# Kernel optimization log

Measured on AMD Instinct MI355X. Metric: run time of the kernel, lower is better.

## Reference

```python
import jax, jax.numpy as jnp
import numpy as np

N_ENT = 50000
N_USR = 10000
N_NODES = N_ENT + N_USR
D = 64            # entity_dim
AE_H = [128, 32]  # autoencoder hidden dims
CONV = [32, 16]   # graph conv output dims
R = 16            # n_relations
E = 1920000       # n_edges (avg degree 32)
B = 4096          # scoring batch


def setup_inputs() -> dict:
    key = jax.random.key(0)
    ks = jax.random.split(key, 24)
    s = 0.05
    rn = lambda k, shp: jax.random.normal(k, shp, jnp.float32) * s
    inp = {
        # int graph / batch inputs
        "users": jax.random.randint(ks[0], (B,), 0, N_USR),
        "items": jax.random.randint(ks[1], (B,), 0, N_ENT),
        "edge_src": jax.random.randint(ks[2], (E,), 0, N_NODES),
        "edge_dst": jax.random.randint(ks[3], (E,), 0, N_NODES),
        "edge_rel": jax.random.randint(ks[4], (E,), 0, R),
        # embeddings
        "entity_emb": rn(ks[5], (N_ENT, D)),
        "user_emb": rn(ks[6], (N_USR, D)),
        # autoencoder (weights stored [in, out])
        "enc_W0": rn(ks[7], (D, AE_H[0])), "enc_b0": jnp.zeros((AE_H[0],), jnp.float32),
        "enc_W1": rn(ks[8], (AE_H[0], AE_H[1])), "enc_b1": jnp.zeros((AE_H[1],), jnp.float32),
        "dec_W0": rn(ks[9], (AE_H[1], AE_H[0])), "dec_b0": jnp.zeros((AE_H[0],), jnp.float32),
        "dec_W1": rn(ks[10], (AE_H[0], D)), "dec_b1": jnp.zeros((D,), jnp.float32),
        # conv layer 1: input_dim=32 -> W_r [R, 64, 32], linear [64 -> 32]
        "Wr1": rn(ks[11], (R, 2 * CONV[0], CONV[0])),
        "lin_W1": rn(ks[12], (2 * CONV[0], CONV[0])), "lin_b1": jnp.zeros((CONV[0],), jnp.float32),
        # conv layer 2: input_dim=32 -> W_r [R, 64, 32], linear [64 -> 16]
        "Wr2": rn(ks[13], (R, 2 * CONV[0], CONV[0])),
        "lin_W2": rn(ks[14], (2 * CONV[0], CONV[1])), "lin_b2": jnp.zeros((CONV[1],), jnp.float32),
    }
    return inp


def _graph_conv(x, edge_src, edge_dst, edge_rel, W_r, lin_W, lin_b):
    # gate logit = sum_j (concat(h_dst, h_src) @ W_r[rel])_j
    #            = concat(h_dst, h_src) . W_r[rel].sum(-1)  (exact identity)
    w_sum = W_r.sum(axis=-1)                      # [R, 2*in]
    h_dst = x[edge_dst]                            # [E, in]
    h_src = x[edge_src]                            # [E, in]
    c = jnp.concatenate([h_dst, h_src], axis=-1)   # [E, 2*in]
    gate = jax.nn.sigmoid(jnp.sum(c * w_sum[edge_rel], axis=-1, keepdims=True))  # [E,1]
    weighted = h_src * gate                        # [E, in]
    n = x.shape[0]
    agg_sum = jax.ops.segment_sum(weighted, edge_dst, num_segments=n)           # [N, in]
    cnt = jax.ops.segment_sum(jnp.ones((edge_dst.shape[0], 1), x.dtype), edge_dst, num_segments=n)
    agg = jnp.where(cnt > 0, agg_sum / jnp.maximum(cnt, 1.0), 0.0)              # scatter-mean
    combined = jnp.concatenate([x, agg], axis=-1)  # [N, 2*in]
    return jax.nn.leaky_relu(combined @ lin_W + lin_b, negative_slope=0.01)


def reference(entity_emb, user_emb,
              enc_W0, enc_b0, enc_W1, enc_b1,
              dec_W0, dec_b0, dec_W1, dec_b1,
              Wr1, lin_W1, lin_b1, Wr2, lin_W2, lin_b2,
              users, items, edge_src, edge_dst, edge_rel):
    all_emb = jnp.concatenate([entity_emb, user_emb], axis=0)  # [N, 64]
    # autoencoder: ReLU between layers, none at the end of encode/decode
    encoded = jax.nn.relu(all_emb @ enc_W0 + enc_b0) @ enc_W1 + enc_b1  # [N, 32]
    decoded = jax.nn.relu(encoded @ dec_W0 + dec_b0) @ dec_W1 + dec_b1  # [N, 64]
    ae_loss = jnp.mean((decoded - all_emb) ** 2)

    x1 = _graph_conv(encoded, edge_src, edge_dst, edge_rel, Wr1, lin_W1, lin_b1)  # [N, 32]
    x2 = _graph_conv(x1, edge_src, edge_dst, edge_rel, Wr2, lin_W2, lin_b2)       # [N, 16]
    final = jnp.concatenate([x1, x2], axis=-1)  # [N, 48]

    user_nodes = N_ENT + users
    scores = jnp.sum(final[user_nodes] * final[items], axis=-1)  # [B]
    return scores, ae_loss
```

## Files before the change

kernel.cpp:

```cpp
#include <hip/hip_runtime.h>
#include <hip/hip_fp16.h>
#include <math.h>

#define N_ENT 50000
#define N_USR 10000
#define NN    60000
#define DD    64
#define H0    128
#define ENCD  32
#define RR    16
#define NB    256
#define BSH   8
#define NBU   235

__device__ __forceinline__ float4 ld4(const float* p){ return *reinterpret_cast<const float4*>(p); }
__device__ __forceinline__ void st4(float* p, float4 v){ *reinterpret_cast<float4*>(p) = v; }

__global__ __launch_bounds__(256) void k_wsum(const float* __restrict__ Wr1, const float* __restrict__ Wr2,
                                              float* __restrict__ wsum){
  int i = blockIdx.x*256 + threadIdx.x;
  if (i >= 2*RR*DD) return;
  const float* Wr = (i < RR*DD) ? Wr1 : Wr2;
  int loc = i & (RR*DD - 1);
  const float* p = Wr + (size_t)loc*32;
  float s = 0.f;
  #pragma unroll
  for (int k=0;k<32;k++) s += p[k];
  wsum[i] = s;
}

__global__ __launch_bounds__(512) void k_ae(const float* __restrict__ ent, const float* __restrict__ usr,
    const float* __restrict__ eW0, const float* __restrict__ eb0,
    const float* __restrict__ eW1, const float* __restrict__ eb1,
    const float* __restrict__ dW0c, const float* __restrict__ db0,
    const float* __restrict__ dW1c, const float* __restrict__ db1,
    float* __restrict__ enc, float* __restrict__ loss_out){
  __shared__ float xs[DD][65];
  __shared__ float hs[H0][65];
  __shared__ float es[ENCD][65];
  __shared__ float sred[8];
  int t = threadIdx.x;
  int nl = t & 63;
  int wid = __builtin_amdgcn_readfirstlane(t >> 6);

  {
    int n2 = t >> 3;
    int d0 = (t & 7) * 8;
    int gnode = blockIdx.x*64 + n2;
    if (gnode < NN){
      const float* xr = (gnode < N_ENT) ? ent + (size_t)gnode*DD : usr + (size_t)(gnode-N_ENT)*DD;
      #pragma unroll
      for (int q=0;q<2;q++){
        float4 v = ld4(xr + d0 + 4*q);
        xs[d0+4*q+0][n2]=v.x; xs[d0+4*q+1][n2]=v.y; xs[d0+4*q+2][n2]=v.z; xs[d0+4*q+3][n2]=v.w;
      }
    } else {
      #pragma unroll
      for (int q=0;q<8;q++) xs[d0+q][n2]=0.f;
    }
  }
  __syncthreads();

  {
    int j0 = wid*16;
    float acc[16];
    #pragma unroll
    for (int k=0;k<16;k++) acc[k]=eb0[j0+k];
    #pragma unroll 4
    for (int d=0;d<DD;d++){
      float x = xs[d][nl];
      const float* w = eW0 + (size_t)d*H0 + j0;
      #pragma unroll
      for (int k=0;k<16;k++) acc[k]=fmaf(x,w[k],acc[k]);
    }
    #pragma unroll
    for (int k=0;k<16;k++) hs[j0+k][nl]=fmaxf(acc[k],0.f);
  }
  __syncthreads();

  {
    int k0 = wid*4;
    float acc[4];
    #pragma unroll
    for (int k=0;k<4;k++) acc[k]=eb1[k0+k];
    #pragma unroll 4
    for (int j=0;j<H0;j++){
      float hv = hs[j][nl];
      const float* w = eW1 + (size_t)j*ENCD + k0;
      #pragma unroll
      for (int k=0;k<4;k++) acc[k]=fmaf(hv,w[k],acc[k]);
    }
    #pragma unroll
    for (int k=0;k<4;k++) es[k0+k][nl]=acc[k];
  }
  __syncthreads();

  {
    int n2 = t >> 3;
    int k2 = (t & 7) * 4;
    int gnode = blockIdx.x*64 + n2;
    if (gnode < NN){
      float4 a;
      a.x=es[k2+0][n2]; a.y=es[k2+1][n2]; a.z=es[k2+2][n2]; a.w=es[k2+3][n2];
      st4(enc + (size_t)gnode*ENCD + k2, a);
    }
  }

  {
    int j0 = wid*16;
    float acc[16];
    #pragma unroll
    for (int k=0;k<16;k++) acc[k]=db0[j0+k];
    #pragma unroll 4
    for (int d=0;d<ENCD;d++){
      float x = es[d][nl];
      const float* w = dW0c + (size_t)d*H0 + j0;
      #pragma unroll
      for (int k=0;k<16;k++) acc[k]=fmaf(x,w[k],acc[k]);
    }
    #pragma unroll
    for (int k=0;k<16;k++) hs[j0+k][nl]=fmaxf(acc[k],0.f);
  }
  __syncthreads();

  float part = 0.f;
  {
    int c0 = wid*8;
    float acc[8];
    #pragma unroll
    for (int k=0;k<8;k++) acc[k]=db1[c0+k];
    #pragma unroll 4
    for (int j=0;j<H0;j++){
      float hv = hs[j][nl];
      const float* w = dW1c + (size_t)j*DD + c0;
      #pragma unroll
      for (int k=0;k<8;k++) acc[k]=fmaf(hv,w[k],acc[k]);
    }
    int gnode = blockIdx.x*64 + nl;
    if (gnode < NN){
      #pragma unroll
      for (int k=0;k<8;k++){ float d_ = acc[k]-xs[c0+k][nl]; part = fmaf(d_,d_,part); }
    }
  }
  #pragma unroll
  for (int off=32; off>0; off>>=1) part += __shfl_down(part, off, 64);
  if ((t&63)==0) sred[wid] = part;
  __syncthreads();
  if (t==0){
    float s = 0.f;
    #pragma unroll
    for (int k=0;k<8;k++) s += sred[k];
    atomicAdd(loss_out, s * (1.0f/((float)NN*(float)DD)));
  }
}

__global__ __launch_bounds__(256) void k_hist256(const int* __restrict__ edst, int* __restrict__ bktCnt, int E_){
  __shared__ int h[NB];
  h[threadIdx.x]=0;
  __syncthreads();
  int i0 = blockIdx.x*4096;
  #pragma unroll
  for (int k=0;k<16;k++){
    int e = i0 + k*256 + threadIdx.x;
    if (e < E_) atomicAdd(&h[((unsigned)edst[e])>>BSH], 1);
  }
  __syncthreads();
  int c = h[threadIdx.x];
  if (c) atomicAdd(&bktCnt[threadIdx.x], c);
}

__global__ __launch_bounds__(256) void k_scan256(const int* __restrict__ bktCnt, int* __restrict__ bktBase){
  __shared__ int wps[4];
  int t = threadIdx.x;
  int v = bktCnt[t];
  int x = v;
  #pragma unroll
  for (int off=1; off<64; off<<=1){
    int y = __shfl_up(x, off, 64);
    if ((t & 63) >= off) x += y;
  }
  if ((t & 63) == 63) wps[t >> 6] = x;
  __syncthreads();
  if (t < 4){
    int wv = wps[t];
    int wx = wv;
    #pragma unroll
    for (int off=1; off<4; off<<=1){
      int y = __shfl_up(wx, off, 4);
      if (t >= off) wx += y;
    }
    wps[t] = wx - wv;
  }
  __syncthreads();
  bktBase[t] = (x - v) + wps[t >> 6];
}

__global__ __launch_bounds__(256) void k_bucketA(const int* __restrict__ esrc, const int* __restrict__ edst,
    const int* __restrict__ erel, const int* __restrict__ bktBase, int* __restrict__ bktFill,
    unsigned* __restrict__ bktData, int E_){
  __shared__ int h[NB];
  __shared__ int gbase[NB];
  h[threadIdx.x]=0;
  __syncthreads();
  int i0 = blockIdx.x*4096;
  int dcache[16];
  #pragma unroll
  for (int k=0;k<16;k++){
    int e = i0 + k*256 + threadIdx.x;
    int d = (e < E_) ? edst[e] : -1;
    dcache[k] = d;
    if (d >= 0) atomicAdd(&h[((unsigned)d)>>BSH], 1);
  }
  __syncthreads();
  {
    int c = h[threadIdx.x];
    int off = c ? atomicAdd(&bktFill[threadIdx.x], c) : 0;
    gbase[threadIdx.x] = bktBase[threadIdx.x] + off;
    h[threadIdx.x] = 0;
  }
  __syncthreads();
  #pragma unroll
  for (int k=0;k<16;k++){
    int e = i0 + k*256 + threadIdx.x;
    if (e >= E_) continue;
    int d = dcache[k];
    int b = ((unsigned)d) >> BSH;
    int slot = atomicAdd(&h[b], 1);
    unsigned rec = (unsigned)esrc[e] | ((unsigned)erel[e] << 16) | ((unsigned)(d & 0xFF) << 20);
    bktData[(size_t)gbase[b] + slot] = rec;
  }
}

__global__ __launch_bounds__(256) void k_buildB(const unsigned* __restrict__ bktData,
    const int* __restrict__ bktBase, const int* __restrict__ bktCnt,
    int* __restrict__ rowp, int* __restrict__ packed){
  __shared__ int cnt[NB];
  __shared__ int start[NB];
  __shared__ int wps[4];
  int b = blockIdx.x;
  int base = bktBase[b];
  int n = bktCnt[b];
  int t = threadIdx.x;
  cnt[t] = 0;
  __syncthreads();
  for (int i=t; i<n; i+=256) atomicAdd(&cnt[(bktData[base+i] >> 20) & 0xFF], 1);
  __syncthreads();
  int v = cnt[t];
  cnt[t] = 0;
  int x = v;
  #pragma unroll
  for (int off=1; off<64; off<<=1){
    int y = __shfl_up(x, off, 64);
    if ((t & 63) >= off) x += y;
  }
  if ((t & 63) == 63) wps[t >> 6] = x;
  __syncthreads();
  if (t < 4){
    int wv = wps[t];
    int wx = wv;
    #pragma unroll
    for (int off=1; off<4; off<<=1){
      int y = __shfl_up(wx, off, 4);
      if (t >= off) wx += y;
    }
    wps[t] = wx - wv;
  }
  __syncthreads();
  int sv = (x - v) + wps[t >> 6];
  start[t] = sv;
  int node = (b << BSH) + t;
  if (node <= NN) rowp[node] = base + sv;
  __syncthreads();
  for (int i=t; i<n; i+=256){
    unsigned r = bktData[base+i];
    int dl = (r >> 20) & 0xFF;
    int p = start[dl] + atomicAdd(&cnt[dl], 1);
    packed[base + p] = (int)r;
  }
}

__global__ __launch_bounds__(256) void k_dots(const float* __restrict__ x, const float* __restrict__ wsum,
    float* __restrict__ dA, __half* __restrict__ dbrec, __half* __restrict__ xrec){
  __shared__ float wl[RR*DD];
  for (int i = threadIdx.x; i < RR*DD; i += 256){
    int r = i & 15; int j = i >> 4;
    wl[i] = wsum[r*DD + j];
  }
  __syncthreads();
  int t = blockIdx.x*256 + threadIdx.x;
  if (t >= NN*RR) return;
  int n = t >> 4, r = t & 15;
  const float* xr = x + (size_t)n*ENCD;
  float a = 0.f, b = 0.f;
  float xlo = 0.f, xhi = 0.f;
  #pragma unroll
  for (int q=0;q<8;q++){
    float4 v = ld4(xr + 4*q);
    int j = 4*q;
    if (r >= j && r < j+4){ float tmp[4]={v.x,v.y,v.z,v.w}; xlo = tmp[r-j]; }
    if (r+16 >= j && r+16 < j+4){ float tmp[4]={v.x,v.y,v.z,v.w}; xhi = tmp[r+16-j]; }
    a = fmaf(v.x, wl[(j+0)*16 + r], a);
    a = fmaf(v.y, wl[(j+1)*16 + r], a);
    a = fmaf(v.z, wl[(j+2)*16 + r], a);
    a = fmaf(v.w, wl[(j+3)*16 + r], a);
    b = fmaf(v.x, wl[(32+j+0)*16 + r], b);
    b = fmaf(v.y, wl[(32+j+1)*16 + r], b);
    b = fmaf(v.z, wl[(32+j+2)*16 + r], b);
    b = fmaf(v.w, wl[(32+j+3)*16 + r], b);
  }
  dA[t] = a;
  dbrec[t] = __float2half(b);
  xrec[(size_t)n*32 + r]      = __float2half(xlo);
  xrec[(size_t)n*32 + 16 + r] = __float2half(xhi);
}

__global__ __launch_bounds__(256) void k_gates(const int* __restrict__ packed,
    const int* __restrict__ bktBase, const int* __restrict__ bktCnt,
    const float* __restrict__ dA, const __half* __restrict__ dbrec, __half* __restrict__ gat){
  int b = blockIdx.x >> 2, g = blockIdx.x & 3;
  int base = bktBase[b], n = bktCnt[b];
  int lo = (n*g) >> 2, hi = (n*(g+1)) >> 2;
  for (int i = lo + (int)threadIdx.x; i < hi; i += 256){
    int p = packed[base+i];
    int s = p & 0xFFFF;
    int r = (p >> 16) & 15;
    int dl = (p >> 20) & 0xFF;
    int dst = (b << BSH) | dl;
    float z = dA[dst*16 + r] + __half2float(dbrec[s*16 + r]);
    gat[base+i] = __float2half(1.f/(1.f + __expf(-z)));
  }
}

__global__ __launch_bounds__(256) void k_agg(const __half2* __restrict__ xrec2, const int* __restrict__ packed,
    const __half* __restrict__ gat, const int* __restrict__ rowp, float* __restrict__ agg){
  int node = blockIdx.x*16 + (threadIdx.x >> 4);
  int l = threadIdx.x & 15;
  if (node >= NN) return;
  int beg = rowp[node], end = rowp[node+1];
  float ax = 0.f, ay = 0.f;
  #pragma unroll 4
  for (int i = beg; i < end; i++){
    int p = packed[i];
    int s = p & 0xFFFF;
    float g = __half2float(gat[i]);
    float2 fx = __half22float2(xrec2[(size_t)s*16 + l]);
    ax = fmaf(fx.x, g, ax);
    ay = fmaf(fx.y, g, ay);
  }
  int deg = end - beg;
  float inv = (deg > 0) ? 1.f/(float)deg : 0.f;
  float2 o; o.x = ax*inv; o.y = ay*inv;
  *reinterpret_cast<float2*>(&agg[(size_t)node*ENCD + 2*l]) = o;
}

__global__ __launch_bounds__(256) void k_lin(const float* __restrict__ x, const float* __restrict__ agg,
    const float* __restrict__ W, const float* __restrict__ b, float* __restrict__ out, int outd){
  int n = blockIdx.x*256 + threadIdx.x;
  if (n >= NN) return;
  int k0 = blockIdx.y * 16;
  const float* xr = x   + (size_t)n*ENCD;
  const float* ar = agg + (size_t)n*ENCD;
  float xv[32], av[32];
  #pragma unroll
  for (int q=0;q<8;q++){ float4 v = ld4(xr+4*q); xv[4*q]=v.x; xv[4*q+1]=v.y; xv[4*q+2]=v.z; xv[4*q+3]=v.w; }
  #pragma unroll
  for (int q=0;q<8;q++){ float4 v = ld4(ar+4*q); av[4*q]=v.x; av[4*q+1]=v.y; av[4*q+2]=v.z; av[4*q+3]=v.w; }
  float acc[16];
  #pragma unroll
  for (int t=0;t<16;t++) acc[t] = b[k0+t];
  #pragma unroll
  for (int j=0;j<32;j++){
    #pragma unroll
    for (int t=0;t<16;t++) acc[t] = fmaf(xv[j], W[(size_t)j*outd + k0 + t], acc[t]);
  }
  #pragma unroll
  for (int j=0;j<32;j++){
    #pragma unroll
    for (int t=0;t<16;t++) acc[t] = fmaf(av[j], W[(size_t)(32+j)*outd + k0 + t], acc[t]);
  }
  float* o = out + (size_t)n*outd + k0;
  #pragma unroll
  for (int q=0;q<4;q++){
    float4 v;
    float a0=acc[4*q],a1=acc[4*q+1],a2=acc[4*q+2],a3=acc[4*q+3];
    v.x = a0>0.f? a0 : 0.01f*a0;
    v.y = a1>0.f? a1 : 0.01f*a1;
    v.z = a2>0.f? a2 : 0.01f*a2;
    v.w = a3>0.f? a3 : 0.01f*a3;
    st4(o + 4*q, v);
  }
}

__global__ __launch_bounds__(256) void k_score(const float* __restrict__ x1, const float* __restrict__ x2,
    const int* __restrict__ users, const int* __restrict__ items, float* __restrict__ out, int Bn){
  int b = blockIdx.x*256 + threadIdx.x;
  if (b >= Bn) return;
  int u  = N_ENT + users[b];
  int it = items[b];
  const float* a1 = x1 + (size_t)u*32;
  const float* c1 = x1 + (size_t)it*32;
  const float* a2 = x2 + (size_t)u*16;
  const float* c2 = x2 + (size_t)it*16;
  float s = 0.f;
  #pragma unroll
  for (int q=0;q<8;q++){
    float4 va=ld4(a1+4*q), vb=ld4(c1+4*q);
    s = fmaf(va.x,vb.x,s); s = fmaf(va.y,vb.y,s); s = fmaf(va.z,vb.z,s); s = fmaf(va.w,vb.w,s);
  }
  #pragma unroll
  for (int q=0;q<4;q++){
    float4 va=ld4(a2+4*q), vb=ld4(c2+4*q);
    s = fmaf(va.x,vb.x,s); s = fmaf(va.y,vb.y,s); s = fmaf(va.z,vb.z,s); s = fmaf(va.w,vb.w,s);
  }
  out[b] = s;
}

extern "C" void kernel_launch(void* const* d_in, const int* in_sizes, int n_in,
                              void* d_out, int out_size, void* d_ws, size_t ws_size,
                              hipStream_t stream){
  const int*   users   = (const int*)d_in[0];
  const int*   items   = (const int*)d_in[1];
  const int*   esrc    = (const int*)d_in[2];
  const int*   edst    = (const int*)d_in[3];
  const int*   erel    = (const int*)d_in[4];
  const float* ent     = (const float*)d_in[5];
  const float* usr     = (const float*)d_in[6];
  const float* enc_W0  = (const float*)d_in[7];
  const float* enc_b0  = (const float*)d_in[8];
  const float* enc_W1  = (const float*)d_in[9];
  const float* enc_b1  = (const float*)d_in[10];
  const float* dec_W0  = (const float*)d_in[11];
  const float* dec_b0  = (const float*)d_in[12];
  const float* dec_W1  = (const float*)d_in[13];
  const float* dec_b1  = (const float*)d_in[14];
  const float* Wr1     = (const float*)d_in[15];
  const float* lin_W1  = (const float*)d_in[16];
  const float* lin_b1  = (const float*)d_in[17];
  const float* Wr2     = (const float*)d_in[18];
  const float* lin_W2  = (const float*)d_in[19];
  const float* lin_b2  = (const float*)d_in[20];
  const int E = in_sizes[2];
  const int B = in_sizes[0];

  char* wp = (char*)d_ws;
  auto carve = [&](size_t bytes)->char*{ char* p = wp; wp += (bytes + 255) & ~(size_t)255; return p; };
  float* enc    = (float*)carve((size_t)NN*32*4);
  float* x1     = (float*)carve((size_t)NN*32*4);
  float* x2     = (float*)carve((size_t)NN*16*4);
  float* agg    = (float*)carve((size_t)NN*32*4);
  float* wsum   = (float*)carve((size_t)2*RR*DD*4);
  float* dA     = (float*)carve((size_t)NN*RR*4);
  __half* dbrec = (__half*)carve((size_t)NN*RR*2);
  __half* xrec  = (__half*)carve((size_t)NN*32*2);
  __half* gat   = (__half*)carve((size_t)E*2);
  int*   packed = (int*)  carve((size_t)E*4);
  unsigned* bktData = (unsigned*)carve((size_t)E*4);
  int*   bktCnt = (int*)  carve((size_t)2*NB*4);
  int*   bktFill= bktCnt + NB;
  int*   bktBase= (int*)  carve(NB*4);
  int*   rowp   = (int*)  carve(((size_t)NN+1)*4);

  const int nbN = (NN + 255)/256;
  const int nbT = (E + 4095)/4096;
  const int nbD = (NN*RR + 255)/256;
  dim3 blk(256);

  hipMemsetAsync(d_out, 0, (size_t)out_size*sizeof(float), stream);
  hipMemsetAsync(bktCnt, 0, (size_t)2*NB*sizeof(int), stream);

  k_wsum <<<dim3((2*RR*DD+255)/256), blk, 0, stream>>>(Wr1, Wr2, wsum);
  k_ae   <<<dim3((NN+63)/64), dim3(512), 0, stream>>>(ent, usr, enc_W0, enc_b0, enc_W1, enc_b1,
                                                      dec_W0, dec_b0, dec_W1, dec_b1,
                                                      enc, ((float*)d_out) + B);

  k_hist256<<<nbT, blk, 0, stream>>>(edst, bktCnt, E);
  k_scan256<<<1, blk, 0, stream>>>(bktCnt, bktBase);
  k_bucketA<<<nbT, blk, 0, stream>>>(esrc, edst, erel, bktBase, bktFill, bktData, E);
  k_buildB <<<NBU, blk, 0, stream>>>(bktData, bktBase, bktCnt, rowp, packed);

  k_dots <<<nbD, blk, 0, stream>>>(enc, wsum, dA, dbrec, xrec);
  k_gates<<<NBU*4, blk, 0, stream>>>(packed, bktBase, bktCnt, dA, dbrec, gat);
  k_agg  <<<(NN+15)/16, blk, 0, stream>>>((const __half2*)xrec, packed, gat, rowp, agg);
  k_lin  <<<dim3(nbN, 2), blk, 0, stream>>>(enc, agg, lin_W1, lin_b1, x1, 32);

  k_dots <<<nbD, blk, 0, stream>>>(x1, wsum + RR*DD, dA, dbrec, xrec);
  k_gates<<<NBU*4, blk, 0, stream>>>(packed, bktBase, bktCnt, dA, dbrec, gat);
  k_agg  <<<(NN+15)/16, blk, 0, stream>>>((const __half2*)xrec, packed, gat, rowp, agg);
  k_lin  <<<dim3(nbN, 1), blk, 0, stream>>>(x1, agg, lin_W2, lin_b2, x2, 16);

  k_score<<<(B+255)/256, blk, 0, stream>>>(x1, x2, users, items, (float*)d_out, B);
}
```

Measured before the change: 383.2 us.

## Fuse histogram and weight-sum into autoencoder launch; split aggregation across half-warps

Merges the edge-destination histogram and relation weight-sum kernels into the autoencoder kernel as extra blocks, removing two launches and letting the independent work run concurrently. The autoencoder now reads input rows directly from global memory instead of staging them in shared memory, which frees LDS so more blocks can be resident. The aggregation kernel assigns 32 lanes per node, with two half-groups each taking alternate edges and combining through a shuffle, to expose more memory-level parallelism per node. The risks are redundant global reads of the embedding rows and one fewer row-per-lane trade-off in the aggregation.

```diff
diff --git a/kernel.cpp b/kernel.cpp
--- a/kernel.cpp
+++ b/kernel.cpp
@@ -16,62 +16,77 @@
 __device__ __forceinline__ float4 ld4(const float* p){ return *reinterpret_cast<const float4*>(p); }
 __device__ __forceinline__ void st4(float* p, float4 v){ *reinterpret_cast<float4*>(p) = v; }
 
-__global__ __launch_bounds__(256) void k_wsum(const float* __restrict__ Wr1, const float* __restrict__ Wr2,
-                                              float* __restrict__ wsum){
-  int i = blockIdx.x*256 + threadIdx.x;
-  if (i >= 2*RR*DD) return;
-  const float* Wr = (i < RR*DD) ? Wr1 : Wr2;
-  int loc = i & (RR*DD - 1);
-  const float* p = Wr + (size_t)loc*32;
-  float s = 0.f;
-  #pragma unroll
-  for (int k=0;k<32;k++) s += p[k];
-  wsum[i] = s;
-}
-
-__global__ __launch_bounds__(512) void k_ae(const float* __restrict__ ent, const float* __restrict__ usr,
+__global__ __launch_bounds__(512, 6) void k_ae_hist(const float* __restrict__ ent, const float* __restrict__ usr,
     const float* __restrict__ eW0, const float* __restrict__ eb0,
     const float* __restrict__ eW1, const float* __restrict__ eb1,
     const float* __restrict__ dW0c, const float* __restrict__ db0,
     const float* __restrict__ dW1c, const float* __restrict__ db1,
-    float* __restrict__ enc, float* __restrict__ loss_out){
-  __shared__ float xs[DD][65];
+    float* __restrict__ enc, float* __restrict__ loss_out,
+    const int* __restrict__ edst, int* __restrict__ bktCnt,
+    const float* __restrict__ Wr1, const float* __restrict__ Wr2, float* __restrict__ wsum,
+    int E_, int nbAE, int nbTh){
   __shared__ float hs[H0][65];
   __shared__ float es[ENCD][65];
   __shared__ float sred[8];
+  int bid = blockIdx.x;
   int t = threadIdx.x;
+
+  if (bid >= nbAE){
+    int rb = bid - nbAE;
+    if (rb < nbTh){
+      int* hh = (int*)&hs[0][0];
+      if (t < NB) hh[t] = 0;
+      __syncthreads();
+      int i0 = rb*8192;
+      #pragma unroll
+      for (int k=0;k<16;k++){
+        int e = i0 + k*512 + t;
+        if (e < E_) atomicAdd(&hh[((unsigned)edst[e])>>BSH], 1);
+      }
+      __syncthreads();
+      if (t < NB){ int c = hh[t]; if (c) atomicAdd(&bktCnt[t], c); }
+    } else {
+      int i = (rb - nbTh)*512 + t;
+      if (i < 2*RR*DD){
+        const float* Wr = (i < RR*DD) ? Wr1 : Wr2;
+        int loc = i & (RR*DD - 1);
+        const float* p = Wr + (size_t)loc*32;
+        float s = 0.f;
+        #pragma unroll
+        for (int k=0;k<32;k++) s += p[k];
+        wsum[i] = s;
+      }
+    }
+    return;
+  }
+
   int nl = t & 63;
   int wid = __builtin_amdgcn_readfirstlane(t >> 6);
-
-  {
-    int n2 = t >> 3;
-    int d0 = (t & 7) * 8;
-    int gnode = blockIdx.x*64 + n2;
-    if (gnode < NN){
-      const float* xr = (gnode < N_ENT) ? ent + (size_t)gnode*DD : usr + (size_t)(gnode-N_ENT)*DD;
-      #pragma unroll
-      for (int q=0;q<2;q++){
-        float4 v = ld4(xr + d0 + 4*q);
-        xs[d0+4*q+0][n2]=v.x; xs[d0+4*q+1][n2]=v.y; xs[d0+4*q+2][n2]=v.z; xs[d0+4*q+3][n2]=v.w;
-      }
-    } else {
-      #pragma unroll
-      for (int q=0;q<8;q++) xs[d0+q][n2]=0.f;
-    }
-  }
-  __syncthreads();
+  int gnode = bid*64 + nl;
+  bool valid = gnode < NN;
+  const float* xr = valid ? ((gnode < N_ENT) ? ent + (size_t)gnode*DD
+                                             : usr + (size_t)(gnode-N_ENT)*DD)
+                          : ent;
 
   {
     int j0 = wid*16;
     float acc[16];
     #pragma unroll
     for (int k=0;k<16;k++) acc[k]=eb0[j0+k];
-    #pragma unroll 4
-    for (int d=0;d<DD;d++){
-      float x = xs[d][nl];
-      const float* w = eW0 + (size_t)d*H0 + j0;
-      #pragma unroll
-      for (int k=0;k<16;k++) acc[k]=fmaf(x,w[k],acc[k]);
+    #pragma unroll
+    for (int dc=0; dc<DD; dc+=16){
+      float xv[16];
+      #pragma unroll
+      for (int q=0;q<4;q++){
+        float4 v = ld4(xr + dc + 4*q);
+        xv[4*q]=v.x; xv[4*q+1]=v.y; xv[4*q+2]=v.z; xv[4*q+3]=v.w;
+      }
+      #pragma unroll
+      for (int dd=0; dd<16; dd++){
+        const float* w = eW0 + (size_t)(dc+dd)*H0 + j0;
+        #pragma unroll
+        for (int k=0;k<16;k++) acc[k]=fmaf(xv[dd], w[k], acc[k]);
+      }
     }
     #pragma unroll
     for (int k=0;k<16;k++) hs[j0+k][nl]=fmaxf(acc[k],0.f);
@@ -98,11 +113,11 @@
   {
     int n2 = t >> 3;
     int k2 = (t & 7) * 4;
-    int gnode = blockIdx.x*64 + n2;
-    if (gnode < NN){
+    int gn2 = bid*64 + n2;
+    if (gn2 < NN){
       float4 a;
       a.x=es[k2+0][n2]; a.y=es[k2+1][n2]; a.z=es[k2+2][n2]; a.w=es[k2+3][n2];
-      st4(enc + (size_t)gnode*ENCD + k2, a);
+      st4(enc + (size_t)gn2*ENCD + k2, a);
     }
   }
 
@@ -136,10 +151,13 @@
       #pragma unroll
       for (int k=0;k<8;k++) acc[k]=fmaf(hv,w[k],acc[k]);
     }
-    int gnode = blockIdx.x*64 + nl;
-    if (gnode < NN){
-      #pragma unroll
-      for (int k=0;k<8;k++){ float d_ = acc[k]-xs[c0+k][nl]; part = fmaf(d_,d_,part); }
+    if (valid){
+      float xl[8];
+      float4 v0 = ld4(xr + c0), v1 = ld4(xr + c0 + 4);
+      xl[0]=v0.x; xl[1]=v0.y; xl[2]=v0.z; xl[3]=v0.w;
+      xl[4]=v1.x; xl[5]=v1.y; xl[6]=v1.z; xl[7]=v1.w;
+      #pragma unroll
+      for (int k=0;k<8;k++){ float d_ = acc[k]-xl[k]; part = fmaf(d_,d_,part); }
     }
   }
   #pragma unroll
@@ -152,21 +170,6 @@
     for (int k=0;k<8;k++) s += sred[k];
     atomicAdd(loss_out, s * (1.0f/((float)NN*(float)DD)));
   }
-}
-
-__global__ __launch_bounds__(256) void k_hist256(const int* __restrict__ edst, int* __restrict__ bktCnt, int E_){
-  __shared__ int h[NB];
-  h[threadIdx.x]=0;
-  __syncthreads();
-  int i0 = blockIdx.x*4096;
-  #pragma unroll
-  for (int k=0;k<16;k++){
-    int e = i0 + k*256 + threadIdx.x;
-    if (e < E_) atomicAdd(&h[((unsigned)edst[e])>>BSH], 1);
-  }
-  __syncthreads();
-  int c = h[threadIdx.x];
-  if (c) atomicAdd(&bktCnt[threadIdx.x], c);
 }
 
 __global__ __launch_bounds__(256) void k_scan256(const int* __restrict__ bktCnt, int* __restrict__ bktBase){
@@ -333,24 +336,30 @@
 
 __global__ __launch_bounds__(256) void k_agg(const __half2* __restrict__ xrec2, const int* __restrict__ packed,
     const __half* __restrict__ gat, const int* __restrict__ rowp, float* __restrict__ agg){
-  int node = blockIdx.x*16 + (threadIdx.x >> 4);
-  int l = threadIdx.x & 15;
+  int node = blockIdx.x*8 + (threadIdx.x >> 5);
+  int l = threadIdx.x & 31;
+  int half = l >> 4;
+  int l16 = l & 15;
   if (node >= NN) return;
   int beg = rowp[node], end = rowp[node+1];
   float ax = 0.f, ay = 0.f;
-  #pragma unroll 4
-  for (int i = beg; i < end; i++){
+  #pragma unroll 2
+  for (int i = beg + half; i < end; i += 2){
     int p = packed[i];
     int s = p & 0xFFFF;
     float g = __half2float(gat[i]);
-    float2 fx = __half22float2(xrec2[(size_t)s*16 + l]);
+    float2 fx = __half22float2(xrec2[(size_t)s*16 + l16]);
     ax = fmaf(fx.x, g, ax);
     ay = fmaf(fx.y, g, ay);
   }
-  int deg = end - beg;
-  float inv = (deg > 0) ? 1.f/(float)deg : 0.f;
-  float2 o; o.x = ax*inv; o.y = ay*inv;
-  *reinterpret_cast<float2*>(&agg[(size_t)node*ENCD + 2*l]) = o;
+  ax += __shfl_xor(ax, 16, 32);
+  ay += __shfl_xor(ay, 16, 32);
+  if (half == 0){
+    int deg = end - beg;
+    float inv = (deg > 0) ? 1.f/(float)deg : 0.f;
+    float2 o; o.x = ax*inv; o.y = ay*inv;
+    *reinterpret_cast<float2*>(&agg[(size_t)node*ENCD + 2*l16]) = o;
+  }
 }
 
 __global__ __launch_bounds__(256) void k_lin(const float* __restrict__ x, const float* __restrict__ agg,
@@ -460,32 +469,32 @@
   int*   bktBase= (int*)  carve(NB*4);
   int*   rowp   = (int*)  carve(((size_t)NN+1)*4);
 
-  const int nbN = (NN + 255)/256;
-  const int nbT = (E + 4095)/4096;
-  const int nbD = (NN*RR + 255)/256;
+  const int nbN  = (NN + 255)/256;
+  const int nbT  = (E + 4095)/4096;
+  const int nbTh = (E + 8191)/8192;
+  const int nbAE = (NN + 63)/64;
+  const int nbD  = (NN*RR + 255)/256;
   dim3 blk(256);
 
   hipMemsetAsync(d_out, 0, (size_t)out_size*sizeof(float), stream);
   hipMemsetAsync(bktCnt, 0, (size_t)2*NB*sizeof(int), stream);
 
-  k_wsum <<<dim3((2*RR*DD+255)/256), blk, 0, stream>>>(Wr1, Wr2, wsum);
-  k_ae   <<<dim3((NN+63)/64), dim3(512), 0, stream>>>(ent, usr, enc_W0, enc_b0, enc_W1, enc_b1,
-                                                      dec_W0, dec_b0, dec_W1, dec_b1,
-                                                      enc, ((float*)d_out) + B);
-
-  k_hist256<<<nbT, blk, 0, stream>>>(edst, bktCnt, E);
+  k_ae_hist<<<dim3(nbAE + nbTh + 4), dim3(512), 0, stream>>>(
+      ent, usr, enc_W0, enc_b0, enc_W1, enc_b1, dec_W0, dec_b0, dec_W1, dec_b1,
+      enc, ((float*)d_out) + B, edst, bktCnt, Wr1, Wr2, wsum, E, nbAE, nbTh);
+
   k_scan256<<<1, blk, 0, stream>>>(bktCnt, bktBase);
   k_bucketA<<<nbT, blk, 0, stream>>>(esrc, edst, erel, bktBase, bktFill, bktData, E);
   k_buildB <<<NBU, blk, 0, stream>>>(bktData, bktBase, bktCnt, rowp, packed);
 
   k_dots <<<nbD, blk, 0, stream>>>(enc, wsum, dA, dbrec, xrec);
   k_gates<<<NBU*4, blk, 0, stream>>>(packed, bktBase, bktCnt, dA, dbrec, gat);
-  k_agg  <<<(NN+15)/16, blk, 0, stream>>>((const __half2*)xrec, packed, gat, rowp, agg);
+  k_agg  <<<(NN+7)/8, blk, 0, stream>>>((const __half2*)xrec, packed, gat, rowp, agg);
   k_lin  <<<dim3(nbN, 2), blk, 0, stream>>>(enc, agg, lin_W1, lin_b1, x1, 32);
 
   k_dots <<<nbD, blk, 0, stream>>>(x1, wsum + RR*DD, dA, dbrec, xrec);
   k_gates<<<NBU*4, blk, 0, stream>>>(packed, bktBase, bktCnt, dA, dbrec, gat);
-  k_agg  <<<(NN+15)/16, blk, 0, stream>>>((const __half2*)xrec, packed, gat, rowp, agg);
+  k_agg  <<<(NN+7)/8, blk, 0, stream>>>((const __half2*)xrec, packed, gat, rowp, agg);
   k_lin  <<<dim3(nbN, 1), blk, 0, stream>>>(x1, agg, lin_W2, lin_b2, x2, 16);
 
   k_score<<<(B+255)/256, blk, 0, stream>>>(x1, x2, users, items, (float*)d_out, B);
```

Measured after the change: 388.6 us. About the same (+1.4%).
